# Optimization experiments

Hardware: AMD Instinct MI355X
Metric: run time of the kernel (lower is better)

Reference implementation:

```python
import jax, jax.numpy as jnp
import numpy as np

B = 32768        # batch
S = 256          # subnet_num
H1, H2 = 10, 6   # subnet_arch
L2_SMOOTH = 1e-3
EPS = 1e-10


def setup_inputs() -> dict:
    key = jax.random.key(0)
    k = jax.random.split(key, 7)
    def glorot(kk, shape, fan_in, fan_out):
        return (jax.random.normal(kk, shape, jnp.float32)
                * np.float32(np.sqrt(2.0 / (fan_in + fan_out))))
    x = jax.random.normal(k[0], (B, S), jnp.float32)
    W1 = glorot(k[1], (S, 1, H1), 1, H1)
    b1 = jnp.zeros((S, H1), jnp.float32)
    W2 = glorot(k[2], (S, H1, H2), H1, H2)
    b2 = jnp.zeros((S, H2), jnp.float32)
    W3 = glorot(k[3], (S, H2, 1), H2, 1)
    b3 = jnp.zeros((S, 1), jnp.float32)
    return {"x": x, "W1": W1, "b1": b1, "W2": W2, "b2": b2, "W3": W3, "b3": b3}


def _mlp_scalar(xs, W1, b1, W2, b2, W3, b3):
    # xs: scalar input of one subnet for one sample
    h = jnp.tanh(xs * W1[0] + b1)   # [H1]
    h = jnp.tanh(h @ W2 + b2)       # [H2]
    return (h @ W3 + b3)[0]         # scalar


def _per_subnet(fn):
    # inner vmap over batch (x axis 0, params broadcast), outer over subnets
    inner = jax.vmap(fn, in_axes=(0, None, None, None, None, None, None))
    return jax.vmap(inner, in_axes=(1, 0, 0, 0, 0, 0, 0))  # -> [S, B]


def reference(x, W1, b1, W2, b2, W3, b3):
    out = _per_subnet(_mlp_scalar)(x, W1, b1, W2, b2, W3, b3)           # [S, B]
    d2f = jax.grad(jax.grad(_mlp_scalar))                               # Hessian diag (scalar input)
    g2 = _per_subnet(d2f)(x, W1, b1, W2, b2, W3, b3)                    # [S, B]
    # training-mode batch stats (population std, as tf.math.reduce_std)
    mean = jnp.mean(out, axis=1, keepdims=True)                         # [S, 1]
    std = jnp.maximum(jnp.std(out, axis=1, keepdims=True), EPS)         # [S, 1]
    out_bn = ((out - mean) / std).T                                     # [B, S]
    smooth_loss = L2_SMOOTH * jnp.sum(jnp.mean(g2 * g2, axis=1) / std[:, 0])
    return out_bn, smooth_loss
```

## Files before the change

kernel.cpp:

```cpp
#include <hip/hip_runtime.h>
#include <math.h>

#define B 32768
#define S 256
#define H1 10
#define H2 6
#define NB 1024
#define L2_SMOOTH 1e-3f
#define EPS 1e-10f

__device__ __forceinline__ void tanh_pair(float x, float& th, float& s2) {
    const float e = __builtin_amdgcn_exp2f(x * 2.885390081777927f);
    const float r = __builtin_amdgcn_rcpf(e + 1.0f);
    th = fmaf(-2.0f, r, 1.0f);
    s2 = (4.0f * r) * (1.0f - r);
}

__global__ __launch_bounds__(256, 3) void k1_mlp(
    const float* __restrict__ x,
    const float* __restrict__ W1, const float* __restrict__ b1,
    const float* __restrict__ W2, const float* __restrict__ b2,
    const float* __restrict__ W3, const float* __restrict__ b3,
    float* __restrict__ out,
    float* __restrict__ psum,
    float* __restrict__ psum2,
    float* __restrict__ pg2)
{
    const int s   = threadIdx.x;
    const int blk = blockIdx.x;
    const int CHUNK = B / NB;

    float w1[H1], bb1[H1], w2[H1][H2], bb2[H2], w3[H2], bb3;
#pragma unroll
    for (int i = 0; i < H1; ++i) { w1[i] = W1[s * H1 + i]; bb1[i] = b1[s * H1 + i]; }
#pragma unroll
    for (int i = 0; i < H1; ++i)
#pragma unroll
        for (int j = 0; j < H2; ++j) w2[i][j] = W2[(s * H1 + i) * H2 + j];
#pragma unroll
    for (int j = 0; j < H2; ++j) { bb2[j] = b2[s * H2 + j]; w3[j] = W3[s * H2 + j]; }
    bb3 = b3[s];

    float so = 0.0f, so2 = 0.0f, sg2 = 0.0f;
    const int b0 = blk * CHUNK;

    for (int bi = 0; bi < CHUNK; ++bi) {
        const int b = b0 + bi;
        const float xs = x[b * S + s];

        float v[H2], vp[H2], vpp[H2];
#pragma unroll
        for (int j = 0; j < H2; ++j) { v[j] = bb2[j]; vp[j] = 0.0f; vpp[j] = 0.0f; }

#pragma unroll
        for (int i = 0; i < H1; ++i) {
            float h, t;
            tanh_pair(fmaf(xs, w1[i], bb1[i]), h, t);
            const float hp  = t * w1[i];
            const float hpp = -2.0f * (h * hp) * w1[i];
#pragma unroll
            for (int j = 0; j < H2; ++j) {
                v[j]   = fmaf(h,   w2[i][j], v[j]);
                vp[j]  = fmaf(hp,  w2[i][j], vp[j]);
                vpp[j] = fmaf(hpp, w2[i][j], vpp[j]);
            }
        }

        float o = bb3, g2 = 0.0f;
#pragma unroll
        for (int j = 0; j < H2; ++j) {
            float g, tg;
            tanh_pair(v[j], g, tg);
            const float c   = -2.0f * (g * vp[j]);
            const float gpp = tg * fmaf(c, vp[j], vpp[j]);
            o  = fmaf(g,     w3[j], o);
            g2 = fmaf(w3[j], gpp,   g2);
        }

        out[b * S + s] = o;
        so  += o;
        so2  = fmaf(o,  o,  so2);
        sg2  = fmaf(g2, g2, sg2);
    }

    psum [blk * S + s] = so;
    psum2[blk * S + s] = so2;
    pg2  [blk * S + s] = sg2;
}

__global__ __launch_bounds__(256) void k2_reduce(
    const float* __restrict__ psum, const float* __restrict__ psum2,
    const float* __restrict__ pg2,
    float* __restrict__ mean_arr, float* __restrict__ rstd_arr,
    float* __restrict__ smooth_arr, int nb)
{
    const int s = blockIdx.x;
    const int t = threadIdx.x;

    float a = 0.0f, b_ = 0.0f, c = 0.0f;
    for (int k = t; k < nb; k += 256) {
        a  += psum [k * S + s];
        b_ += psum2[k * S + s];
        c  += pg2  [k * S + s];
    }

    __shared__ float sa[256], sb[256], sc[256];
    sa[t] = a; sb[t] = b_; sc[t] = c;
    __syncthreads();
    for (int st = 128; st > 0; st >>= 1) {
        if (t < st) { sa[t] += sa[t + st]; sb[t] += sb[t + st]; sc[t] += sc[t + st]; }
        __syncthreads();
    }

    if (t == 0) {
        const float inv_b = 1.0f / (float)B;
        const float mean  = sa[0] * inv_b;
        float var = sb[0] * inv_b - mean * mean;
        var = fmaxf(var, 0.0f);
        const float stdv = fmaxf(sqrtf(var), EPS);
        const float rstd = 1.0f / stdv;
        mean_arr[s]   = mean;
        rstd_arr[s]   = rstd;
        smooth_arr[s] = (sc[0] * inv_b) * rstd;
    }
}

#define K3_NORM_BLOCKS (B * S / (256 * 4))
__global__ __launch_bounds__(256) void k3_norm(
    float* __restrict__ out,
    const float* __restrict__ mean_arr, const float* __restrict__ rstd_arr,
    const float* __restrict__ smooth_arr)
{
    if ((int)blockIdx.x == K3_NORM_BLOCKS) {
        const int t = threadIdx.x;
        __shared__ float sa[256];
        sa[t] = smooth_arr[t];
        __syncthreads();
        for (int st = 128; st > 0; st >>= 1) {
            if (t < st) sa[t] += sa[t + st];
            __syncthreads();
        }
        if (t == 0) out[B * S] = L2_SMOOTH * sa[0];
        return;
    }

    const int i4   = (int)blockIdx.x * 256 + (int)threadIdx.x;
    const int base = i4 * 4;
    float4 v = *reinterpret_cast<float4*>(&out[base]);
    const int s0 = base & (S - 1);
    v.x = (v.x - mean_arr[s0 + 0]) * rstd_arr[s0 + 0];
    v.y = (v.y - mean_arr[s0 + 1]) * rstd_arr[s0 + 1];
    v.z = (v.z - mean_arr[s0 + 2]) * rstd_arr[s0 + 2];
    v.w = (v.w - mean_arr[s0 + 3]) * rstd_arr[s0 + 3];
    *reinterpret_cast<float4*>(&out[base]) = v;
}

extern "C" void kernel_launch(void* const* d_in, const int* in_sizes, int n_in,
                              void* d_out, int out_size, void* d_ws, size_t ws_size,
                              hipStream_t stream) {
    const float* x  = (const float*)d_in[0];
    const float* W1 = (const float*)d_in[1];
    const float* b1 = (const float*)d_in[2];
    const float* W2 = (const float*)d_in[3];
    const float* b2 = (const float*)d_in[4];
    const float* W3 = (const float*)d_in[5];
    const float* b3 = (const float*)d_in[6];
    float* out = (float*)d_out;

    float* psum   = (float*)d_ws;
    float* psum2  = psum  + NB * S;
    float* pg2    = psum2 + NB * S;
    float* meanA  = pg2   + NB * S;
    float* rstdA  = meanA + S;
    float* smooth = rstdA + S;

    k1_mlp<<<NB, 256, 0, stream>>>(x, W1, b1, W2, b2, W3, b3, out, psum, psum2, pg2);
    k2_reduce<<<S, 256, 0, stream>>>(psum, psum2, pg2, meanA, rstdA, smooth, NB);
    k3_norm<<<K3_NORM_BLOCKS + 1, 256, 0, stream>>>(out, meanA, rstdA, smooth);
}
```

Measured before the change: 121.4 us.

## Map subnets to wavefronts with batch lanes and stage x/out through LDS

Restructures the MLP kernel so each wavefront handles one subnet and its 64 lanes cover batch samples. Subnet weights become wave-uniform via readfirstlane, which lets them sit in scalar registers. Input tiles are loaded as float4 into padded LDS and transposed back for coalesced output stores. Partial stats are reduced with wave shuffles into a smaller subnet-major workspace that k2 reads directly. This aims to cut vector register pressure and raise occupancy, at the cost of extra LDS traffic and block-wide barriers.

```diff
diff --git a/kernel.cpp b/kernel.cpp
--- a/kernel.cpp
+++ b/kernel.cpp
@@ -5,9 +5,17 @@
 #define S 256
 #define H1 10
 #define H2 6
-#define NB 1024
+#define ST 16
+#define CB 1024
+#define RB 256
+#define PAD 20
+#define NCHUNK (B / CB)
 #define L2_SMOOTH 1e-3f
 #define EPS 1e-10f
+
+__device__ __forceinline__ float rfl(float x) {
+    return __int_as_float(__builtin_amdgcn_readfirstlane(__float_as_int(x)));
+}
 
 __device__ __forceinline__ void tanh_pair(float x, float& th, float& s2) {
     const float e = __builtin_amdgcn_exp2f(x * 2.885390081777927f);
@@ -16,7 +24,7 @@
     s2 = (4.0f * r) * (1.0f - r);
 }
 
-__global__ __launch_bounds__(256, 3) void k1_mlp(
+__global__ __launch_bounds__(1024, 4) void k1_mlp(
     const float* __restrict__ x,
     const float* __restrict__ W1, const float* __restrict__ b1,
     const float* __restrict__ W2, const float* __restrict__ b2,
@@ -26,82 +34,110 @@
     float* __restrict__ psum2,
     float* __restrict__ pg2)
 {
-    const int s   = threadIdx.x;
-    const int blk = blockIdx.x;
-    const int CHUNK = B / NB;
-
-    float w1[H1], bb1[H1], w2[H1][H2], bb2[H2], w3[H2], bb3;
+    __shared__ float xlds[RB * PAD];
+    __shared__ float olds[RB * PAD];
+
+    const int t  = threadIdx.x;
+    const int wv = __builtin_amdgcn_readfirstlane(t >> 6);
+    const int l  = t & 63;
+    const int s0 = blockIdx.x * ST;
+    const int s  = s0 + wv;
+    const int bbase = blockIdx.y * CB;
+
+    float w1[H1], bb1[H1], w2s[H1][H2], bb2[H2], w3[H2];
 #pragma unroll
     for (int i = 0; i < H1; ++i) { w1[i] = W1[s * H1 + i]; bb1[i] = b1[s * H1 + i]; }
 #pragma unroll
     for (int i = 0; i < H1; ++i)
 #pragma unroll
-        for (int j = 0; j < H2; ++j) w2[i][j] = W2[(s * H1 + i) * H2 + j];
-#pragma unroll
-    for (int j = 0; j < H2; ++j) { bb2[j] = b2[s * H2 + j]; w3[j] = W3[s * H2 + j]; }
-    bb3 = b3[s];
+        for (int j = 0; j < H2; ++j) w2s[i][j] = rfl(W2[(s * H1 + i) * H2 + j]);
+#pragma unroll
+    for (int j = 0; j < H2; ++j) { bb2[j] = rfl(b2[s * H2 + j]); w3[j] = rfl(W3[s * H2 + j]); }
+    const float bb3 = rfl(b3[s]);
+    float w1m2[H1];
+#pragma unroll
+    for (int i = 0; i < H1; ++i) w1m2[i] = -2.0f * w1[i] * w1[i];
+
+    const int brow = t >> 2;
+    const int s4   = (t & 3) * 4;
 
     float so = 0.0f, so2 = 0.0f, sg2 = 0.0f;
-    const int b0 = blk * CHUNK;
-
-    for (int bi = 0; bi < CHUNK; ++bi) {
-        const int b = b0 + bi;
-        const float xs = x[b * S + s];
-
-        float v[H2], vp[H2], vpp[H2];
-#pragma unroll
-        for (int j = 0; j < H2; ++j) { v[j] = bb2[j]; vp[j] = 0.0f; vpp[j] = 0.0f; }
-
-#pragma unroll
-        for (int i = 0; i < H1; ++i) {
-            float h, t;
-            tanh_pair(fmaf(xs, w1[i], bb1[i]), h, t);
-            const float hp  = t * w1[i];
-            const float hpp = -2.0f * (h * hp) * w1[i];
+
+    for (int r = 0; r < CB / RB; ++r) {
+        const float4 xv = *reinterpret_cast<const float4*>(
+            &x[(bbase + r * RB + brow) * S + s0 + s4]);
+        *reinterpret_cast<float4*>(&xlds[brow * PAD + s4]) = xv;
+        __syncthreads();
+
+#pragma unroll
+        for (int k = 0; k < RB / 64; ++k) {
+            const float xs = xlds[(k * 64 + l) * PAD + wv];
+
+            float v[H2], vp[H2], vpp[H2];
+#pragma unroll
+            for (int j = 0; j < H2; ++j) { v[j] = bb2[j]; vp[j] = 0.0f; vpp[j] = 0.0f; }
+
+#pragma unroll
+            for (int i = 0; i < H1; ++i) {
+                float h, tt;
+                tanh_pair(fmaf(xs, w1[i], bb1[i]), h, tt);
+                const float hp  = tt * w1[i];
+                const float hpp = (h * tt) * w1m2[i];
+#pragma unroll
+                for (int j = 0; j < H2; ++j) {
+                    v[j]   = fmaf(h,   w2s[i][j], v[j]);
+                    vp[j]  = fmaf(hp,  w2s[i][j], vp[j]);
+                    vpp[j] = fmaf(hpp, w2s[i][j], vpp[j]);
+                }
+            }
+
+            float o = bb3, g2 = 0.0f;
 #pragma unroll
             for (int j = 0; j < H2; ++j) {
-                v[j]   = fmaf(h,   w2[i][j], v[j]);
-                vp[j]  = fmaf(hp,  w2[i][j], vp[j]);
-                vpp[j] = fmaf(hpp, w2[i][j], vpp[j]);
+                float g, tg;
+                tanh_pair(v[j], g, tg);
+                const float c   = -2.0f * (g * vp[j]);
+                const float gpp = tg * fmaf(c, vp[j], vpp[j]);
+                o  = fmaf(g,     w3[j], o);
+                g2 = fmaf(w3[j], gpp,   g2);
             }
+
+            olds[(k * 64 + l) * PAD + wv] = o;
+            so += o; so2 = fmaf(o, o, so2); sg2 = fmaf(g2, g2, sg2);
         }
-
-        float o = bb3, g2 = 0.0f;
-#pragma unroll
-        for (int j = 0; j < H2; ++j) {
-            float g, tg;
-            tanh_pair(v[j], g, tg);
-            const float c   = -2.0f * (g * vp[j]);
-            const float gpp = tg * fmaf(c, vp[j], vpp[j]);
-            o  = fmaf(g,     w3[j], o);
-            g2 = fmaf(w3[j], gpp,   g2);
-        }
-
-        out[b * S + s] = o;
-        so  += o;
-        so2  = fmaf(o,  o,  so2);
-        sg2  = fmaf(g2, g2, sg2);
-    }
-
-    psum [blk * S + s] = so;
-    psum2[blk * S + s] = so2;
-    pg2  [blk * S + s] = sg2;
+        __syncthreads();
+
+        const float4 ov = *reinterpret_cast<const float4*>(&olds[brow * PAD + s4]);
+        *reinterpret_cast<float4*>(&out[(bbase + r * RB + brow) * S + s0 + s4]) = ov;
+    }
+
+#pragma unroll
+    for (int m = 1; m < 64; m <<= 1) {
+        so  += __shfl_xor(so,  m, 64);
+        so2 += __shfl_xor(so2, m, 64);
+        sg2 += __shfl_xor(sg2, m, 64);
+    }
+    if (l == 0) {
+        psum [s * NCHUNK + blockIdx.y] = so;
+        psum2[s * NCHUNK + blockIdx.y] = so2;
+        pg2  [s * NCHUNK + blockIdx.y] = sg2;
+    }
 }
 
 __global__ __launch_bounds__(256) void k2_reduce(
     const float* __restrict__ psum, const float* __restrict__ psum2,
     const float* __restrict__ pg2,
     float* __restrict__ mean_arr, float* __restrict__ rstd_arr,
-    float* __restrict__ smooth_arr, int nb)
+    float* __restrict__ smooth_arr)
 {
     const int s = blockIdx.x;
     const int t = threadIdx.x;
 
     float a = 0.0f, b_ = 0.0f, c = 0.0f;
-    for (int k = t; k < nb; k += 256) {
-        a  += psum [k * S + s];
-        b_ += psum2[k * S + s];
-        c  += pg2  [k * S + s];
+    if (t < NCHUNK) {
+        a  = psum [s * NCHUNK + t];
+        b_ = psum2[s * NCHUNK + t];
+        c  = pg2  [s * NCHUNK + t];
     }
 
     __shared__ float sa[256], sb[256], sc[256];
@@ -168,13 +204,14 @@
     float* out = (float*)d_out;
 
     float* psum   = (float*)d_ws;
-    float* psum2  = psum  + NB * S;
-    float* pg2    = psum2 + NB * S;
-    float* meanA  = pg2   + NB * S;
+    float* psum2  = psum  + S * NCHUNK;
+    float* pg2    = psum2 + S * NCHUNK;
+    float* meanA  = pg2   + S * NCHUNK;
     float* rstdA  = meanA + S;
     float* smooth = rstdA + S;
 
-    k1_mlp<<<NB, 256, 0, stream>>>(x, W1, b1, W2, b2, W3, b3, out, psum, psum2, pg2);
-    k2_reduce<<<S, 256, 0, stream>>>(psum, psum2, pg2, meanA, rstdA, smooth, NB);
+    k1_mlp<<<dim3(S / ST, NCHUNK), 1024, 0, stream>>>(
+        x, W1, b1, W2, b2, W3, b3, out, psum, psum2, pg2);
+    k2_reduce<<<S, 256, 0, stream>>>(psum, psum2, pg2, meanA, rstdA, smooth);
     k3_norm<<<K3_NORM_BLOCKS + 1, 256, 0, stream>>>(out, meanA, rstdA, smooth);
 }
```

Measured after the change: 120.3 us. About the same (-0.9%).
